# Optimization experiments

Measured on AMD Instinct MI355X. Metric: run time of the kernel, lower is better.

The kernel has to match this reference:

```python
import jax, jax.numpy as jnp
import numpy as np

V, E, H, C = 50000, 300, 512, 3
B, P_LEN, H_LEN = 64, 128, 64


def _lstm(x, Wih, Whh, bih, bhh, h0, c0):
    """torch-style LSTM (gate order i,f,g,o). x: [B,T,E] -> outputs [B,T,H], hT, cT."""
    def step(carry, xt):
        h, c = carry
        g = xt @ Wih.T + h @ Whh.T + bih + bhh  # [B,4H]
        i, f, gg, o = jnp.split(g, 4, axis=-1)
        c = jax.nn.sigmoid(f) * c + jax.nn.sigmoid(i) * jnp.tanh(gg)
        h = jax.nn.sigmoid(o) * jnp.tanh(c)
        return (h, c), h
    (hT, cT), ys = jax.lax.scan(step, (h0, c0), jnp.swapaxes(x, 0, 1))
    return jnp.swapaxes(ys, 0, 1), hT, cT


def setup_inputs() -> dict:
    key = jax.random.key(0)
    ks = iter(jax.random.split(key, 32))
    n = lambda shape, s=0.05: jax.random.normal(next(ks), shape, dtype=jnp.float32) * s
    inp = {
        "premise": jax.random.randint(next(ks), (B, P_LEN), 0, V, dtype=jnp.int32),
        "hypothesis": jax.random.randint(next(ks), (B, H_LEN), 0, V, dtype=jnp.int32),
        "emb": n((V, E), 0.1),
        "Wih1": n((4 * H, E)), "Whh1": n((4 * H, H)), "bih1": n((4 * H,)), "bhh1": n((4 * H,)),
        "Wih2": n((4 * H, E)), "Whh2": n((4 * H, H)), "bih2": n((4 * H,)), "bhh2": n((4 * H,)),
        "W_y": n((H, H)), "W_h": n((H, H)), "W_r": n((H, H)), "W_t": n((H, H)),
        "w_att": n((1, H)),
        "fc1_w": n((H, H)), "fc1_b": n((H,)),
        "fc2_w": n((H, H)), "fc2_b": n((H,)),
        "fc3_w": n((C, H)), "fc3_b": n((C,)),
    }
    return inp


def reference(premise, hypothesis, emb,
              Wih1, Whh1, bih1, bhh1,
              Wih2, Whh2, bih2, bhh2,
              W_y, W_h, W_r, W_t, w_att,
              fc1_w, fc1_b, fc2_w, fc2_b, fc3_w, fc3_b):
    Bsz = premise.shape[0]
    Hd = Whh1.shape[1]
    zeros = jnp.zeros((Bsz, Hd), jnp.float32)

    # premise LSTM
    xp = emb[premise]                                   # [B,P,E]
    out_p, _, c_p = _lstm(xp, Wih1, Whh1, bih1, bhh1, zeros, zeros)
    # hypothesis LSTM initialized with (h0=0, c0=c_p)
    xh = emb[hypothesis]                                # [B,Th,E]
    out_h, hn_h, _ = _lstm(xh, Wih2, Whh2, bih2, bhh2, zeros, c_p)

    # word-by-word attention: a1 = W_y @ V^T, fixed across steps
    a1 = jnp.einsum('hj,bpj->bhp', W_y, out_p)          # [B,H,P]
    wv = w_att[0]                                       # [H]

    def att_step(r, q_t):
        # r: [B,H] attention state; q_t: [B,H] hypothesis step
        a2 = q_t @ W_h.T + r @ W_r.T                    # [B,H]
        s = jnp.einsum('h,bhp->bp', wv, jnp.tanh(a1 + a2[:, :, None]))
        scores = jax.nn.softmax(s, axis=-1)             # over premise positions
        r = jnp.einsum('bph,bp->bh', out_p, scores) + jnp.tanh(r @ W_t.T)
        return r, None

    r, _ = jax.lax.scan(att_step, zeros, jnp.swapaxes(out_h, 0, 1))

    rep = jnp.tanh(r @ fc1_w.T + fc1_b + hn_h @ fc2_w.T + fc2_b)
    return rep @ fc3_w.T + fc3_b                         # [B,C]
```

## Files before the change

kernel.cpp:

```cpp
#include <hip/hip_runtime.h>
#include <math.h>

#define BSZ 64
#define PLEN 128
#define HLEN 64
#define EDIM 300
#define HDIM 512
#define G4 2048
#define NCLS 3

#define SPIN_CAP (1 << 18)

#define CR16 576
#define C16(f) ((((f) >> 5) * 36) + ((f) & 31))

__device__ __forceinline__ float sigf(float x) { return 1.0f / (1.0f + __expf(-x)); }
__device__ __forceinline__ float tanhfast(float x) { return 1.0f - 2.0f / (__expf(2.0f * x) + 1.0f); }

__device__ __forceinline__ unsigned long long aload64(const unsigned long long* p) {
    return __hip_atomic_load(p, __ATOMIC_RELAXED, __HIP_MEMORY_SCOPE_AGENT);
}
__device__ __forceinline__ void astore64(unsigned long long* p, unsigned long long v) {
    __hip_atomic_store(p, v, __ATOMIC_RELAXED, __HIP_MEMORY_SCOPE_AGENT);
}
__device__ __forceinline__ unsigned long long fpack2(float lo, float hi) {
    float2 v = make_float2(lo, hi);
    return *(unsigned long long*)&v;
}
__device__ __forceinline__ float2 funpack2(unsigned long long u) {
    union { unsigned long long u; float2 f; } c; c.u = u; return c.f;
}

__global__ __launch_bounds__(256) void ws_zero(unsigned long long* p) {
    p[(size_t)blockIdx.x * 256 + threadIdx.x] = 0ull;
}

__global__ __launch_bounds__(256) void proj_kernel(
    const int* __restrict__ toks, const float* __restrict__ emb,
    const float* __restrict__ Wih, const float* __restrict__ bih,
    const float* __restrict__ bhh, float* __restrict__ out)
{
    __shared__ float es[32 * 100];
    __shared__ float wsh[64 * 100];
    __shared__ int tks[32];
    const int m0 = blockIdx.x * 32, r0 = blockIdx.y * 64;
    const int tid = threadIdx.x;
    const int tx = tid & 15, ty = tid >> 4;
    float acc[2][4] = {{0.f, 0.f, 0.f, 0.f}, {0.f, 0.f, 0.f, 0.f}};
    if (tid < 32) tks[tid] = toks[m0 + tid];
    __syncthreads();
    for (int kc = 0; kc < 3; kc++) {
        if (kc) __syncthreads();
        for (int i = tid; i < 800; i += 256) {
            int row = i / 25, k4 = i % 25;
            ((float4*)es)[i] = ((const float4*)(emb + (size_t)tks[row] * EDIM + kc * 100))[k4];
        }
        for (int i = tid; i < 1600; i += 256) {
            int row = i / 25, k4 = i % 25;
            ((float4*)wsh)[i] = ((const float4*)(Wih + (size_t)(r0 + row) * EDIM + kc * 100))[k4];
        }
        __syncthreads();
        const float4* e0 = (const float4*)es + ty * 25;
        const float4* e1 = e0 + 16 * 25;
        const float4* w0 = (const float4*)wsh + tx * 25;
#pragma unroll
        for (int k = 0; k < 25; k++) {
            float4 ea = e0[k], eb = e1[k];
#pragma unroll
            for (int j = 0; j < 4; j++) {
                float4 w = w0[k + j * 400];
                acc[0][j] += ea.x * w.x + ea.y * w.y + ea.z * w.z + ea.w * w.w;
                acc[1][j] += eb.x * w.x + eb.y * w.y + eb.z * w.z + eb.w * w.w;
            }
        }
    }
#pragma unroll
    for (int j = 0; j < 4; j++) {
        int rr = r0 + tx + j * 16;
        float bsum = bih[rr] + bhh[rr];
        out[(size_t)(m0 + ty) * G4 + rr]      = acc[0][j] + bsum;
        out[(size_t)(m0 + ty + 16) * G4 + rr] = acc[1][j] + bsum;
    }
}

__global__ __launch_bounds__(256, 1) void lstm_coop(
    const float* __restrict__ xp, const float* __restrict__ xh,
    const float* __restrict__ Whh1, const float* __restrict__ Whh2,
    float* __restrict__ outp, float* __restrict__ outh,
    unsigned long long* __restrict__ hA, unsigned long long* __restrict__ hB,
    unsigned long long* __restrict__ hC, unsigned long long* __restrict__ hD,
    unsigned long long* __restrict__ doneH)
{
    const int tid = threadIdx.x;
    const int ug = blockIdx.x >> 3;
    const int bg = blockIdx.x & 7;
    const int u0 = ug * 16, b0 = bg * 8;
    const int rq = tid >> 4, cc = tid & 15;

    __shared__ __align__(16) float hst[8 * CR16];
    __shared__ float gsm[64][9];

    float4 w4[32];
#pragma unroll
    for (int j = 0; j < 4; j++) {
        int rr = 4 * rq + j;
        const float4* src = (const float4*)(Whh1 +
            ((size_t)((rr >> 4) * HDIM + u0 + (rr & 15))) * HDIM) + cc * 8;
#pragma unroll
        for (int q = 0; q < 8; q++) w4[j * 8 + q] = src[q];
    }
    float creg = 0.0f;
    const int bbc = tid >> 4, uuc = tid & 15;
    unsigned long long* dn = doneH + bg * 32;

    for (int t = 0; t < PLEN + HLEN; t++) {
        const int layer2 = (t >= PLEN) ? 1 : 0;
        const int tloc = layer2 ? t - PLEN : t;
        const int T = layer2 ? HLEN : PLEN;
        const float* xproj = layer2 ? xh : xp;
        float* outseq = layer2 ? outh : outp;
        unsigned long long* wA = layer2 ? hC : hA;
        unsigned long long* wB = layer2 ? hD : hB;
        unsigned long long* hwr = (t & 1) ? wB : wA;
        const unsigned long long* hrd = (t & 1) ? wA : wB;

        float gi = 0.f, gf = 0.f, gg = 0.f, go = 0.f;
        if (tid < 128) {
            size_t xb = ((size_t)(b0 + bbc) * T + tloc) * G4 + u0 + uuc;
            gi = xproj[xb];        gf = xproj[xb + 512];
            gg = xproj[xb + 1024]; go = xproj[xb + 1536];
        }

        if (t == PLEN) {
#pragma unroll
            for (int j = 0; j < 4; j++) {
                int rr = 4 * rq + j;
                const float4* src = (const float4*)(Whh2 +
                    ((size_t)((rr >> 4) * HDIM + u0 + (rr & 15))) * HDIM) + cc * 8;
#pragma unroll
                for (int q = 0; q < 8; q++) w4[j * 8 + q] = src[q];
            }
        }
        const bool have_h = (tloc != 0);
        if (have_h) {
            if (tid < 32) {
                unsigned long long v = aload64(dn + tid);
                int guard = 0;
                while (!__all(v >= (unsigned long long)t)) {
                    if (++guard > SPIN_CAP) break;
                    __builtin_amdgcn_s_sleep(1);
                    if (v < (unsigned long long)t) v = aload64(dn + tid);
                }
            }
            __syncthreads();
            __asm__ volatile("" ::: "memory");
            const unsigned long long* src = hrd + (size_t)b0 * 256;
            unsigned long long v[8];
#pragma unroll
            for (int i = 0; i < 8; i++) v[i] = aload64(src + tid + i * 256);
#pragma unroll
            for (int i = 0; i < 8; i++) {
                int idx = tid + i * 256;
                int bb = idx >> 8, j = idx & 255;
                float2 f = funpack2(v[i]);
                *(float2*)&hst[bb * CR16 + C16(2 * j)] = f;
            }
            __syncthreads();
#pragma unroll 1
            for (int bb = 0; bb < 8; bb++) {
                const float* hb = &hst[bb * CR16 + cc * 36];
                float a0 = 0.f, a1 = 0.f, a2 = 0.f, a3 = 0.f;
#pragma unroll
                for (int q = 0; q < 8; q++) {
                    float4 hv = *(const float4*)(hb + 4 * q);
                    float4 x;
                    x = w4[q];      a0 += x.x * hv.x + x.y * hv.y + x.z * hv.z + x.w * hv.w;
                    x = w4[8 + q];  a1 += x.x * hv.x + x.y * hv.y + x.z * hv.z + x.w * hv.w;
                    x = w4[16 + q]; a2 += x.x * hv.x + x.y * hv.y + x.z * hv.z + x.w * hv.w;
                    x = w4[24 + q]; a3 += x.x * hv.x + x.y * hv.y + x.z * hv.z + x.w * hv.w;
                }
#pragma unroll
                for (int o = 1; o < 16; o <<= 1) {
                    a0 += __shfl_xor(a0, o);
                    a1 += __shfl_xor(a1, o);
                    a2 += __shfl_xor(a2, o);
                    a3 += __shfl_xor(a3, o);
                }
                if (cc == 0) {
                    gsm[4 * rq + 0][bb] = a0;
                    gsm[4 * rq + 1][bb] = a1;
                    gsm[4 * rq + 2][bb] = a2;
                    gsm[4 * rq + 3][bb] = a3;
                }
            }
        }
        __syncthreads();
        float hn = 0.f;
        if (tid < 128) {
            if (have_h) {
                gi += gsm[uuc][bbc];
                gf += gsm[16 + uuc][bbc];
                gg += gsm[32 + uuc][bbc];
                go += gsm[48 + uuc][bbc];
            }
            float cn = sigf(gf) * creg + sigf(gi) * tanhfast(gg);
            hn = sigf(go) * tanhfast(cn);
            creg = cn;
            float pr = __shfl_xor(hn, 1);
            if ((uuc & 1) == 0)
                astore64(hwr + (size_t)(b0 + bbc) * 256 + (u0 + uuc) / 2, fpack2(hn, pr));
        }
        __asm__ volatile("s_waitcnt vmcnt(0)" ::: "memory");
        __syncthreads();
        if (tid == 0) astore64(&dn[ug], (unsigned long long)(t + 1));
        if (tid < 128)
            outseq[((size_t)(b0 + bbc) * T + tloc) * HDIM + u0 + uuc] = hn;
    }
}

__global__ __launch_bounds__(256) void a1_kernel(
    const float* __restrict__ W, const float* __restrict__ src,
    float* __restrict__ dst, int T)
{
    __shared__ float os[32 * 132];
    __shared__ float wsh[64 * 132];
    const int b = blockIdx.x, p0 = blockIdx.y * 32, h0 = blockIdx.z * 64;
    const int tid = threadIdx.x;
    const int tx = tid & 15, ty = tid >> 4;
    float acc[2][4] = {{0.f, 0.f, 0.f, 0.f}, {0.f, 0.f, 0.f, 0.f}};
    for (int kc = 0; kc < 4; kc++) {
        if (kc) __syncthreads();
        for (int i = tid; i < 1024; i += 256) {
            int row = i >> 5, k4 = i & 31;
            ((float4*)os)[row * 33 + k4] =
                ((const float4*)(src + ((size_t)(b * T) + p0 + row) * HDIM + kc * 128))[k4];
        }
        for (int i = tid; i < 2048; i += 256) {
            int row = i >> 5, k4 = i & 31;
            ((float4*)wsh)[row * 33 + k4] =
                ((const float4*)(W + (size_t)(h0 + row) * HDIM + kc * 128))[k4];
        }
        __syncthreads();
        const float4* o0 = (const float4*)os + ty * 33;
        const float4* o1 = o0 + 16 * 33;
        const float4* w0 = (const float4*)wsh + tx * 33;
#pragma unroll
        for (int k = 0; k < 32; k++) {
            float4 ea = o0[k], eb = o1[k];
#pragma unroll
            for (int j = 0; j < 4; j++) {
                float4 w = w0[k + j * 528];
                acc[0][j] += ea.x * w.x + ea.y * w.y + ea.z * w.z + ea.w * w.w;
                acc[1][j] += eb.x * w.x + eb.y * w.y + eb.z * w.z + eb.w * w.w;
            }
        }
    }
#pragma unroll
    for (int j = 0; j < 4; j++) {
        int hh = h0 + tx + j * 16;
        dst[((size_t)b * T + p0 + ty) * HDIM + hh]      = acc[0][j];
        dst[((size_t)b * T + p0 + ty + 16) * HDIM + hh] = acc[1][j];
    }
}

#define OSTR 2056
__global__ __launch_bounds__(256, 1) void att_coop2(
    const float* __restrict__ a1b,
    const float* __restrict__ a2qb,
    const float* __restrict__ outp,
    const float* __restrict__ Wr, const float* __restrict__ Wt,
    const float* __restrict__ wv,
    unsigned long long* __restrict__ rA, unsigned long long* __restrict__ rB,
    unsigned long long* __restrict__ sPart,
    unsigned long long* __restrict__ dnS, unsigned long long* __restrict__ dnR)
{
    const int tid = threadIdx.x;
    const int ug = blockIdx.x >> 3;
    const int bg = blockIdx.x & 7;
    const int u0 = ug * 16, b0 = bg * 8;
    const int rp = tid >> 4, cc = tid & 15;
    const int ab = tid >> 5, aq = tid & 31;

    __shared__ __align__(16) float rst[8 * CR16];
    __shared__ __align__(16) float ops[8 * OSTR];
    __shared__ __align__(16) float scst[8][132];
    __shared__ float a2sl[16][9];
    __shared__ float ttsl[16][9];
    __shared__ float wvs[16];

    float4 wr4[8], wt4[8];
    {
        const float4* sr = (const float4*)(Wr + (size_t)(u0 + rp) * HDIM) + cc * 8;
        const float4* st = (const float4*)(Wt + (size_t)(u0 + rp) * HDIM) + cc * 8;
#pragma unroll
        for (int q = 0; q < 8; q++) { wr4[q] = sr[q]; wt4[q] = st[q]; }
    }
    if (tid < 16) wvs[tid] = wv[u0 + tid];

    for (int i = tid; i < 8 * 128 * 4; i += 256) {
        int bb = i >> 9;
        int rem = i & 511;
        int p = rem >> 2, q = rem & 3;
        float4 v = *((const float4*)(outp + ((size_t)(b0 + bb) * PLEN + p) * HDIM + u0) + q);
        *((float4*)(ops + bb * OSTR + p * 16) + q) = v;
    }
    float4 a1r[4][4];
#pragma unroll
    for (int p = 0; p < 4; p++) {
        const float4* src = (const float4*)(a1b +
            ((size_t)(b0 + ab) * PLEN + 4 * aq + p) * HDIM + u0);
#pragma unroll
        for (int k = 0; k < 4; k++) a1r[p][k] = src[k];
    }
    __syncthreads();

    unsigned long long* myS = dnS + bg * 32;
    unsigned long long* myR = dnR + bg * 32;
    const int bbc = tid >> 4, uuc = tid & 15;

    for (int t = 0; t < HLEN; t++) {
        unsigned long long* rwr = (t & 1) ? rB : rA;
        const unsigned long long* rrd = (t & 1) ? rA : rB;
        unsigned long long* sp = sPart + ((size_t)((t & 1) * 8 + bg)) * 16384;

        if (tid < 128) {
            int b = tid >> 4, hh = tid & 15;
            a2sl[hh][b] = a2qb[((size_t)(b0 + b) * HLEN + t) * HDIM + u0 + hh];
            ttsl[hh][b] = 0.f;
        }
        if (t > 0) {
            if (tid < 32) {
                unsigned long long v = aload64(myR + tid);
                int guard = 0;
                while (!__all(v >= (unsigned long long)t)) {
                    if (++guard > SPIN_CAP) break;
                    __builtin_amdgcn_s_sleep(1);
                    if (v < (unsigned long long)t) v = aload64(myR + tid);
                }
            }
            __syncthreads();
            __asm__ volatile("" ::: "memory");
            const unsigned long long* src = rrd + (size_t)b0 * 256;
            unsigned long long v[8];
#pragma unroll
            for (int i = 0; i < 8; i++) v[i] = aload64(src + tid + i * 256);
#pragma unroll
            for (int i = 0; i < 8; i++) {
                int idx = tid + i * 256;
                int bb = idx >> 8, j = idx & 255;
                float2 f = funpack2(v[i]);
                *(float2*)&rst[bb * CR16 + C16(2 * j)] = f;
            }
        }
        __syncthreads();
        if (t > 0) {
#pragma unroll 1
            for (int b = 0; b < 8; b++) {
                const float* hb = &rst[b * CR16 + cc * 36];
                float ar = 0.f, at = 0.f;
#pragma unroll
                for (int q = 0; q < 8; q++) {
                    float4 hv = *(const float4*)(hb + 4 * q);
                    float4 x = wr4[q], y = wt4[q];
                    ar += x.x * hv.x + x.y * hv.y + x.z * hv.z + x.w * hv.w;
                    at += y.x * hv.x + y.y * hv.y + y.z * hv.z + y.w * hv.w;
                }
#pragma unroll
                for (int o = 1; o < 16; o <<= 1) {
                    ar += __shfl_xor(ar, o);
                    at += __shfl_xor(at, o);
                }
                if (cc == 0) {
                    a2sl[rp][b] += ar;
                    ttsl[rp][b] = tanhfast(at);
                }
            }
        }
        __syncthreads();
        {
            float s4[4];
#pragma unroll
            for (int p = 0; p < 4; p++) {
                float s = 0.f;
#pragma unroll
                for (int k = 0; k < 4; k++) {
                    float4 av = a1r[p][k];
                    s += wvs[4 * k + 0] * tanhfast(av.x + a2sl[4 * k + 0][ab])
                       + wvs[4 * k + 1] * tanhfast(av.y + a2sl[4 * k + 1][ab])
                       + wvs[4 * k + 2] * tanhfast(av.z + a2sl[4 * k + 2][ab])
                       + wvs[4 * k + 3] * tanhfast(av.w + a2sl[4 * k + 3][ab]);
                }
                s4[p] = s;
            }
            unsigned long long* d = sp + ((size_t)ug * 8 + ab) * 64 + aq * 2;
            astore64(d, fpack2(s4[0], s4[1]));
            astore64(d + 1, fpack2(s4[2], s4[3]));
        }
        __asm__ volatile("s_waitcnt vmcnt(0)" ::: "memory");
        __syncthreads();
        if (tid == 0) astore64(&myS[ug], (unsigned long long)(t + 1));

        {
            if (tid < 32) {
                unsigned long long v = aload64(myS + tid);
                int guard = 0;
                while (!__all(v >= (unsigned long long)(t + 1))) {
                    if (++guard > SPIN_CAP) break;
                    __builtin_amdgcn_s_sleep(1);
                    if (v < (unsigned long long)(t + 1)) v = aload64(myS + tid);
                }
            }
            __syncthreads();
            __asm__ volatile("" ::: "memory");
#pragma unroll
            for (int i = 0; i < 2; i++) {
                int idx = tid + i * 256;
                int b = idx >> 6, p2 = idx & 63;
                float sx = 0.f, sy = 0.f;
#pragma unroll 8
                for (int g = 0; g < 32; g++) {
                    float2 f = funpack2(aload64(sp + ((size_t)g * 8 + b) * 64 + p2));
                    sx += f.x; sy += f.y;
                }
                scst[b][2 * p2] = sx;
                scst[b][2 * p2 + 1] = sy;
            }
        }
        __syncthreads();
        {
            const int bb = tid >> 5, j = tid & 31;
            float4 v = *(float4*)&scst[bb][j * 4];
            float mx = fmaxf(fmaxf(v.x, v.y), fmaxf(v.z, v.w));
#pragma unroll
            for (int o = 1; o < 32; o <<= 1) mx = fmaxf(mx, __shfl_xor(mx, o));
            float ex = __expf(v.x - mx), ey = __expf(v.y - mx);
            float ez = __expf(v.z - mx), ew = __expf(v.w - mx);
            float ssum = (ex + ey) + (ez + ew);
#pragma unroll
            for (int o = 1; o < 32; o <<= 1) ssum += __shfl_xor(ssum, o);
            float inv = 1.0f / ssum;
            float4 sc4 = make_float4(ex * inv, ey * inv, ez * inv, ew * inv);
            *(float4*)&scst[bb][j * 4] = sc4;
        }
        __syncthreads();
        if (tid < 128) {
            float acc = ttsl[uuc][bbc];
            const float* opb = ops + bbc * OSTR + uuc;
#pragma unroll 8
            for (int p = 0; p < PLEN; p++)
                acc += scst[bbc][p] * opb[p * 16];
            float pr = __shfl_xor(acc, 1);
            if ((uuc & 1) == 0)
                astore64(rwr + (size_t)(b0 + bbc) * 256 + (u0 + uuc) / 2, fpack2(acc, pr));
        }
        __asm__ volatile("s_waitcnt vmcnt(0)" ::: "memory");
        __syncthreads();
        if (tid == 0) astore64(&myR[ug], (unsigned long long)(t + 1));
    }
}

__global__ __launch_bounds__(256) void final_kernel(
    const unsigned long long* __restrict__ r2, const float* __restrict__ outh,
    const float* __restrict__ fc1w, const float* __restrict__ fc1b,
    const float* __restrict__ fc2w, const float* __restrict__ fc2b,
    const float* __restrict__ fc3w, const float* __restrict__ fc3b,
    float* __restrict__ out)
{
    int b = blockIdx.x, tid = threadIdx.x;
    __shared__ float rs[HDIM], hs[HDIM], rep[HDIM], red[256];
    {
        float2 f = funpack2(r2[(size_t)b * 256 + tid]);
        rs[2 * tid] = f.x; rs[2 * tid + 1] = f.y;
    }
    for (int i = tid; i < 128; i += 256)
        ((float4*)hs)[i] = ((const float4*)(outh + ((size_t)(b * HLEN + HLEN - 1)) * HDIM))[i];
    __syncthreads();
    for (int u = tid; u < HDIM; u += 256) {
        const float4* w1 = (const float4*)(fc1w + (size_t)u * HDIM);
        const float4* w2 = (const float4*)(fc2w + (size_t)u * HDIM);
        float a = 0.f, bacc = 0.f;
        for (int k = 0; k < 128; k++) {
            float4 rv = ((float4*)rs)[k], hv = ((float4*)hs)[k];
            float4 x = w1[k]; a    += rv.x * x.x + rv.y * x.y + rv.z * x.z + rv.w * x.w;
            float4 y = w2[k]; bacc += hv.x * y.x + hv.y * y.y + hv.z * y.z + hv.w * y.w;
        }
        rep[u] = tanhfast(a + fc1b[u] + bacc + fc2b[u]);
    }
    __syncthreads();
    for (int cix = 0; cix < NCLS; cix++) {
        red[tid] = rep[tid] * fc3w[(size_t)cix * HDIM + tid]
                 + rep[tid + 256] * fc3w[(size_t)cix * HDIM + tid + 256];
        __syncthreads();
        for (int off = 128; off; off >>= 1) {
            if (tid < off) red[tid] += red[tid + off];
            __syncthreads();
        }
        if (tid == 0) out[b * NCLS + cix] = red[0] + fc3b[cix];
        __syncthreads();
    }
}

extern "C" void kernel_launch(void* const* d_in, const int* in_sizes, int n_in,
                              void* d_out, int out_size, void* d_ws, size_t ws_size,
                              hipStream_t stream)
{
    const int*   premise = (const int*)d_in[0];
    const int*   hyp     = (const int*)d_in[1];
    const float* emb     = (const float*)d_in[2];
    const float* Wih1    = (const float*)d_in[3];
    const float* Whh1    = (const float*)d_in[4];
    const float* bih1    = (const float*)d_in[5];
    const float* bhh1    = (const float*)d_in[6];
    const float* Wih2    = (const float*)d_in[7];
    const float* Whh2    = (const float*)d_in[8];
    const float* bih2    = (const float*)d_in[9];
    const float* bhh2    = (const float*)d_in[10];
    const float* Wy      = (const float*)d_in[11];
    const float* Wh      = (const float*)d_in[12];
    const float* Wr      = (const float*)d_in[13];
    const float* Wt      = (const float*)d_in[14];
    const float* wv      = (const float*)d_in[15];
    const float* fc1w    = (const float*)d_in[16];
    const float* fc1b    = (const float*)d_in[17];
    const float* fc2w    = (const float*)d_in[18];
    const float* fc2b    = (const float*)d_in[19];
    const float* fc3w    = (const float*)d_in[20];
    const float* fc3b    = (const float*)d_in[21];
    float* out = (float*)d_out;

    float* ws = (float*)d_ws;
    size_t off = 0;
    float* xp    = ws + off; off += (size_t)BSZ * PLEN * G4;
    float* xh    = ws + off; off += (size_t)BSZ * HLEN * G4;
    float* outp  = ws + off; off += (size_t)BSZ * PLEN * HDIM;
    float* outhp = ws + off; off += (size_t)BSZ * HLEN * HDIM;
    float* a1b   = ws + off; off += (size_t)BSZ * HDIM * PLEN;
    float* a2qb  = xp;
    unsigned long long* tbase = (unsigned long long*)(ws + off);
    unsigned long long* hAb   = tbase;
    unsigned long long* hBb   = tbase + 16384;
    unsigned long long* hCb   = tbase + 2 * 16384;
    unsigned long long* hDb   = tbase + 3 * 16384;
    unsigned long long* sPart = tbase + 4 * 16384;
    unsigned long long* dnH   = sPart + 262144;
    unsigned long long* dnS   = dnH + 256;
    unsigned long long* dnR   = dnS + 256;
    off += (size_t)(4 * 16384 + 262144 + 768) * 2;
    if (ws_size < off * sizeof(float)) return;

    ws_zero<<<dim3(3), dim3(256), 0, stream>>>(dnH);

    proj_kernel<<<dim3(BSZ * PLEN / 32, G4 / 64), dim3(256), 0, stream>>>(
        premise, emb, Wih1, bih1, bhh1, xp);
    proj_kernel<<<dim3(BSZ * HLEN / 32, G4 / 64), dim3(256), 0, stream>>>(
        hyp, emb, Wih2, bih2, bhh2, xh);

    lstm_coop<<<dim3(256), dim3(256), 0, stream>>>(
        xp, xh, Whh1, Whh2, outp, outhp, hAb, hBb, hCb, hDb, dnH);

    a1_kernel<<<dim3(BSZ, PLEN / 32, HDIM / 64), dim3(256), 0, stream>>>(
        Wy, outp, a1b, PLEN);
    a1_kernel<<<dim3(BSZ, HLEN / 32, HDIM / 64), dim3(256), 0, stream>>>(
        Wh, outhp, a2qb, HLEN);

    att_coop2<<<dim3(256), dim3(256), 0, stream>>>(
        a1b, a2qb, outp, Wr, Wt, wv, hCb, hDb, sPart, dnS, dnR);

    final_kernel<<<dim3(BSZ), dim3(256), 0, stream>>>(
        hDb, outhp, fc1w, fc1b, fc2w, fc2b, fc3w, fc3b, out);
}
```

Baseline: 3.141 ms.

## Halve persistent block count by giving each block 32 hidden units with 512 threads

Both persistent cooperative kernels (LSTM recurrence and attention) now run 128 blocks of 512 threads, each owning 32 hidden units instead of 16. The goal is to halve the number of participants in the per-step cross-block flag synchronisation and the score-partial reduction, cutting spin-wait and global-memory traffic per timestep. In exchange each block does twice the gate and softmax work, uses more LDS, and only half the CUs run, which may serialise more compute per step.

```diff
diff --git a/kernel.cpp b/kernel.cpp
--- a/kernel.cpp
+++ b/kernel.cpp
@@ -83,7 +83,7 @@
     }
 }
 
-__global__ __launch_bounds__(256, 1) void lstm_coop(
+__global__ __launch_bounds__(512, 1) void lstm_coop(
     const float* __restrict__ xp, const float* __restrict__ xh,
     const float* __restrict__ Whh1, const float* __restrict__ Whh2,
     float* __restrict__ outp, float* __restrict__ outh,
@@ -94,24 +94,25 @@
     const int tid = threadIdx.x;
     const int ug = blockIdx.x >> 3;
     const int bg = blockIdx.x & 7;
-    const int u0 = ug * 16, b0 = bg * 8;
+    const int u0 = ug * 32, b0 = bg * 8;
     const int rq = tid >> 4, cc = tid & 15;
 
     __shared__ __align__(16) float hst[8 * CR16];
-    __shared__ float gsm[64][9];
+    __shared__ float gsm[128][9];
 
     float4 w4[32];
 #pragma unroll
     for (int j = 0; j < 4; j++) {
         int rr = 4 * rq + j;
+        int g = rr >> 5, uur = rr & 31;
         const float4* src = (const float4*)(Whh1 +
-            ((size_t)((rr >> 4) * HDIM + u0 + (rr & 15))) * HDIM) + cc * 8;
+            ((size_t)(g * HDIM + u0 + uur)) * HDIM) + cc * 8;
 #pragma unroll
         for (int q = 0; q < 8; q++) w4[j * 8 + q] = src[q];
     }
     float creg = 0.0f;
-    const int bbc = tid >> 4, uuc = tid & 15;
-    unsigned long long* dn = doneH + bg * 32;
+    const int bbc = tid >> 5, uuc = tid & 31;
+    unsigned long long* dn = doneH + bg * 16;
 
     for (int t = 0; t < PLEN + HLEN; t++) {
         const int layer2 = (t >= PLEN) ? 1 : 0;
@@ -125,7 +126,7 @@
         const unsigned long long* hrd = (t & 1) ? wA : wB;
 
         float gi = 0.f, gf = 0.f, gg = 0.f, go = 0.f;
-        if (tid < 128) {
+        if (tid < 256) {
             size_t xb = ((size_t)(b0 + bbc) * T + tloc) * G4 + u0 + uuc;
             gi = xproj[xb];        gf = xproj[xb + 512];
             gg = xproj[xb + 1024]; go = xproj[xb + 1536];
@@ -135,15 +136,16 @@
 #pragma unroll
             for (int j = 0; j < 4; j++) {
                 int rr = 4 * rq + j;
+                int g = rr >> 5, uur = rr & 31;
                 const float4* src = (const float4*)(Whh2 +
-                    ((size_t)((rr >> 4) * HDIM + u0 + (rr & 15))) * HDIM) + cc * 8;
+                    ((size_t)(g * HDIM + u0 + uur)) * HDIM) + cc * 8;
 #pragma unroll
                 for (int q = 0; q < 8; q++) w4[j * 8 + q] = src[q];
             }
         }
         const bool have_h = (tloc != 0);
         if (have_h) {
-            if (tid < 32) {
+            if (tid < 16) {
                 unsigned long long v = aload64(dn + tid);
                 int guard = 0;
                 while (!__all(v >= (unsigned long long)t)) {
@@ -155,12 +157,12 @@
             __syncthreads();
             __asm__ volatile("" ::: "memory");
             const unsigned long long* src = hrd + (size_t)b0 * 256;
-            unsigned long long v[8];
-#pragma unroll
-            for (int i = 0; i < 8; i++) v[i] = aload64(src + tid + i * 256);
-#pragma unroll
-            for (int i = 0; i < 8; i++) {
-                int idx = tid + i * 256;
+            unsigned long long v[4];
+#pragma unroll
+            for (int i = 0; i < 4; i++) v[i] = aload64(src + tid + i * 512);
+#pragma unroll
+            for (int i = 0; i < 4; i++) {
+                int idx = tid + i * 512;
                 int bb = idx >> 8, j = idx & 255;
                 float2 f = funpack2(v[i]);
                 *(float2*)&hst[bb * CR16 + C16(2 * j)] = f;
@@ -196,12 +198,12 @@
         }
         __syncthreads();
         float hn = 0.f;
-        if (tid < 128) {
+        if (tid < 256) {
             if (have_h) {
                 gi += gsm[uuc][bbc];
-                gf += gsm[16 + uuc][bbc];
-                gg += gsm[32 + uuc][bbc];
-                go += gsm[48 + uuc][bbc];
+                gf += gsm[32 + uuc][bbc];
+                gg += gsm[64 + uuc][bbc];
+                go += gsm[96 + uuc][bbc];
             }
             float cn = sigf(gf) * creg + sigf(gi) * tanhfast(gg);
             hn = sigf(go) * tanhfast(cn);
@@ -213,7 +215,7 @@
         __asm__ volatile("s_waitcnt vmcnt(0)" ::: "memory");
         __syncthreads();
         if (tid == 0) astore64(&dn[ug], (unsigned long long)(t + 1));
-        if (tid < 128)
+        if (tid < 256)
             outseq[((size_t)(b0 + bbc) * T + tloc) * HDIM + u0 + uuc] = hn;
     }
 }
@@ -263,8 +265,8 @@
     }
 }
 
-#define OSTR 2056
-__global__ __launch_bounds__(256, 1) void att_coop2(
+#define OSTR2 4104
+__global__ __launch_bounds__(512, 1) void att_coop2(
     const float* __restrict__ a1b,
     const float* __restrict__ a2qb,
     const float* __restrict__ outp,
@@ -277,16 +279,16 @@
     const int tid = threadIdx.x;
     const int ug = blockIdx.x >> 3;
     const int bg = blockIdx.x & 7;
-    const int u0 = ug * 16, b0 = bg * 8;
+    const int u0 = ug * 32, b0 = bg * 8;
     const int rp = tid >> 4, cc = tid & 15;
-    const int ab = tid >> 5, aq = tid & 31;
-
+    const int ab = tid >> 6, aq = tid & 63;
+
+    __shared__ __align__(16) float ops[8 * OSTR2];
     __shared__ __align__(16) float rst[8 * CR16];
-    __shared__ __align__(16) float ops[8 * OSTR];
     __shared__ __align__(16) float scst[8][132];
-    __shared__ float a2sl[16][9];
-    __shared__ float ttsl[16][9];
-    __shared__ float wvs[16];
+    __shared__ float a2sl[32][9];
+    __shared__ float ttsl[32][9];
+    __shared__ float wvs[32];
 
     float4 wr4[8], wt4[8];
     {
@@ -295,41 +297,40 @@
 #pragma unroll
         for (int q = 0; q < 8; q++) { wr4[q] = sr[q]; wt4[q] = st[q]; }
     }
-    if (tid < 16) wvs[tid] = wv[u0 + tid];
-
-    for (int i = tid; i < 8 * 128 * 4; i += 256) {
-        int bb = i >> 9;
-        int rem = i & 511;
-        int p = rem >> 2, q = rem & 3;
+    if (tid < 32) wvs[tid] = wv[u0 + tid];
+
+    for (int i = tid; i < 8192; i += 512) {
+        int bb = i >> 10;
+        int rem = i & 1023;
+        int p = rem >> 3, q = rem & 7;
         float4 v = *((const float4*)(outp + ((size_t)(b0 + bb) * PLEN + p) * HDIM + u0) + q);
-        *((float4*)(ops + bb * OSTR + p * 16) + q) = v;
-    }
-    float4 a1r[4][4];
-#pragma unroll
-    for (int p = 0; p < 4; p++) {
+        *((float4*)(ops + bb * OSTR2 + p * 32) + q) = v;
+    }
+    float4 a1r[2][8];
+#pragma unroll
+    for (int pi = 0; pi < 2; pi++) {
         const float4* src = (const float4*)(a1b +
-            ((size_t)(b0 + ab) * PLEN + 4 * aq + p) * HDIM + u0);
-#pragma unroll
-        for (int k = 0; k < 4; k++) a1r[p][k] = src[k];
+            ((size_t)(b0 + ab) * PLEN + 2 * aq + pi) * HDIM + u0);
+#pragma unroll
+        for (int k = 0; k < 8; k++) a1r[pi][k] = src[k];
     }
     __syncthreads();
 
-    unsigned long long* myS = dnS + bg * 32;
-    unsigned long long* myR = dnR + bg * 32;
-    const int bbc = tid >> 4, uuc = tid & 15;
+    unsigned long long* myS = dnS + bg * 16;
+    unsigned long long* myR = dnR + bg * 16;
+    const int bbc = tid >> 5, uuc = tid & 31;
 
     for (int t = 0; t < HLEN; t++) {
         unsigned long long* rwr = (t & 1) ? rB : rA;
         const unsigned long long* rrd = (t & 1) ? rA : rB;
-        unsigned long long* sp = sPart + ((size_t)((t & 1) * 8 + bg)) * 16384;
-
-        if (tid < 128) {
-            int b = tid >> 4, hh = tid & 15;
-            a2sl[hh][b] = a2qb[((size_t)(b0 + b) * HLEN + t) * HDIM + u0 + hh];
-            ttsl[hh][b] = 0.f;
+        unsigned long long* sp = sPart + ((size_t)((t & 1) * 8 + bg)) * 8192;
+
+        if (tid < 256) {
+            a2sl[uuc][bbc] = a2qb[((size_t)(b0 + bbc) * HLEN + t) * HDIM + u0 + uuc];
+            ttsl[uuc][bbc] = 0.f;
         }
         if (t > 0) {
-            if (tid < 32) {
+            if (tid < 16) {
                 unsigned long long v = aload64(myR + tid);
                 int guard = 0;
                 while (!__all(v >= (unsigned long long)t)) {
@@ -341,12 +342,12 @@
             __syncthreads();
             __asm__ volatile("" ::: "memory");
             const unsigned long long* src = rrd + (size_t)b0 * 256;
-            unsigned long long v[8];
-#pragma unroll
-            for (int i = 0; i < 8; i++) v[i] = aload64(src + tid + i * 256);
-#pragma unroll
-            for (int i = 0; i < 8; i++) {
-                int idx = tid + i * 256;
+            unsigned long long v[4];
+#pragma unroll
+            for (int i = 0; i < 4; i++) v[i] = aload64(src + tid + i * 512);
+#pragma unroll
+            for (int i = 0; i < 4; i++) {
+                int idx = tid + i * 512;
                 int bb = idx >> 8, j = idx & 255;
                 float2 f = funpack2(v[i]);
                 *(float2*)&rst[bb * CR16 + C16(2 * j)] = f;
@@ -378,30 +379,28 @@
         }
         __syncthreads();
         {
-            float s4[4];
-#pragma unroll
-            for (int p = 0; p < 4; p++) {
+            float s2[2];
+#pragma unroll
+            for (int pi = 0; pi < 2; pi++) {
                 float s = 0.f;
 #pragma unroll
-                for (int k = 0; k < 4; k++) {
-                    float4 av = a1r[p][k];
+                for (int k = 0; k < 8; k++) {
+                    float4 av = a1r[pi][k];
                     s += wvs[4 * k + 0] * tanhfast(av.x + a2sl[4 * k + 0][ab])
                        + wvs[4 * k + 1] * tanhfast(av.y + a2sl[4 * k + 1][ab])
                        + wvs[4 * k + 2] * tanhfast(av.z + a2sl[4 * k + 2][ab])
                        + wvs[4 * k + 3] * tanhfast(av.w + a2sl[4 * k + 3][ab]);
                 }
-                s4[p] = s;
-            }
-            unsigned long long* d = sp + ((size_t)ug * 8 + ab) * 64 + aq * 2;
-            astore64(d, fpack2(s4[0], s4[1]));
-            astore64(d + 1, fpack2(s4[2], s4[3]));
+                s2[pi] = s;
+            }
+            astore64(sp + ((size_t)ug * 8 + ab) * 64 + aq, fpack2(s2[0], s2[1]));
         }
         __asm__ volatile("s_waitcnt vmcnt(0)" ::: "memory");
         __syncthreads();
         if (tid == 0) astore64(&myS[ug], (unsigned long long)(t + 1));
 
         {
-            if (tid < 32) {
+            if (tid < 16) {
                 unsigned long long v = aload64(myS + tid);
                 int guard = 0;
                 while (!__all(v >= (unsigned long long)(t + 1))) {
@@ -412,13 +411,11 @@
             }
             __syncthreads();
             __asm__ volatile("" ::: "memory");
-#pragma unroll
-            for (int i = 0; i < 2; i++) {
-                int idx = tid + i * 256;
-                int b = idx >> 6, p2 = idx & 63;
+            {
+                int b = tid >> 6, p2 = tid & 63;
                 float sx = 0.f, sy = 0.f;
-#pragma unroll 8
-                for (int g = 0; g < 32; g++) {
+#pragma unroll 4
+                for (int g = 0; g < 16; g++) {
                     float2 f = funpack2(aload64(sp + ((size_t)g * 8 + b) * 64 + p2));
                     sx += f.x; sy += f.y;
                 }
@@ -427,7 +424,7 @@
             }
         }
         __syncthreads();
-        {
+        if (tid < 256) {
             const int bb = tid >> 5, j = tid & 31;
             float4 v = *(float4*)&scst[bb][j * 4];
             float mx = fmaxf(fmaxf(v.x, v.y), fmaxf(v.z, v.w));
@@ -443,12 +440,12 @@
             *(float4*)&scst[bb][j * 4] = sc4;
         }
         __syncthreads();
-        if (tid < 128) {
+        if (tid < 256) {
             float acc = ttsl[uuc][bbc];
-            const float* opb = ops + bbc * OSTR + uuc;
+            const float* opb = ops + bbc * OSTR2 + uuc;
 #pragma unroll 8
             for (int p = 0; p < PLEN; p++)
-                acc += scst[bbc][p] * opb[p * 16];
+                acc += scst[bbc][p] * opb[p * 32];
             float pr = __shfl_xor(acc, 1);
             if ((uuc & 1) == 0)
                 astore64(rwr + (size_t)(b0 + bbc) * 256 + (u0 + uuc) / 2, fpack2(acc, pr));
@@ -542,10 +539,10 @@
     unsigned long long* hCb   = tbase + 2 * 16384;
     unsigned long long* hDb   = tbase + 3 * 16384;
     unsigned long long* sPart = tbase + 4 * 16384;
-    unsigned long long* dnH   = sPart + 262144;
+    unsigned long long* dnH   = sPart + 131072;
     unsigned long long* dnS   = dnH + 256;
     unsigned long long* dnR   = dnS + 256;
-    off += (size_t)(4 * 16384 + 262144 + 768) * 2;
+    off += (size_t)(4 * 16384 + 131072 + 768) * 2;
     if (ws_size < off * sizeof(float)) return;
 
     ws_zero<<<dim3(3), dim3(256), 0, stream>>>(dnH);
@@ -555,7 +552,7 @@
     proj_kernel<<<dim3(BSZ * HLEN / 32, G4 / 64), dim3(256), 0, stream>>>(
         hyp, emb, Wih2, bih2, bhh2, xh);
 
-    lstm_coop<<<dim3(256), dim3(256), 0, stream>>>(
+    lstm_coop<<<dim3(128), dim3(512), 0, stream>>>(
         xp, xh, Whh1, Whh2, outp, outhp, hAb, hBb, hCb, hDb, dnH);
 
     a1_kernel<<<dim3(BSZ, PLEN / 32, HDIM / 64), dim3(256), 0, stream>>>(
@@ -563,7 +560,7 @@
     a1_kernel<<<dim3(BSZ, HLEN / 32, HDIM / 64), dim3(256), 0, stream>>>(
         Wh, outhp, a2qb, HLEN);
 
-    att_coop2<<<dim3(256), dim3(256), 0, stream>>>(
+    att_coop2<<<dim3(128), dim3(512), 0, stream>>>(
         a1b, a2qb, outp, Wr, Wt, wv, hCb, hDb, sPart, dnS, dnR);
 
     final_kernel<<<dim3(BSZ), dim3(256), 0, stream>>>(
```

After: 3.204 ms. 1.02x slower.
